# Performance work log

Measured on AMD Instinct MI355X. Metric: run time of the kernel, lower is better.

Reference implementation:

```python
import jax, jax.numpy as jnp
import numpy as np

B, N, C = 2, 384, 128
D = C // 4          # bottleneck_dim
H = 128             # time_mlp_hidden_dim


def setup_inputs() -> dict:
    key = jax.random.key(0)
    ks = jax.random.split(key, 12)
    s = 0.02
    return {
        "edge_embed": jax.random.normal(ks[0], (B, N, N, C), jnp.float32),
        "edge_mask": jax.random.randint(ks[1], (B, N, N), 0, 2, jnp.int32),
        "r3_t": jax.random.uniform(ks[2], (B,), jnp.float32),
        # linear params stored as [in, out]
        "Wg": jax.random.normal(ks[3], (C, D), jnp.float32) * s,
        "bg": jnp.zeros((D,), jnp.float32),
        "Wv": jax.random.normal(ks[4], (C, D), jnp.float32) * s,
        "bv": jnp.zeros((D,), jnp.float32),
        "Wd": jax.random.normal(ks[5], (C, D), jnp.float32) * s,
        "bd": jnp.zeros((D,), jnp.float32),
        "Wo": jax.random.normal(ks[6], (D, C), jnp.float32) * s,
        "bo": jnp.zeros((C,), jnp.float32),
        "W1": jax.random.normal(ks[7], (1, H), jnp.float32) * s,
        "b1": jnp.zeros((H,), jnp.float32),
        "W2": jax.random.normal(ks[8], (H, 2 * C), jnp.float32) * s,
        "b2": jnp.zeros((2 * C,), jnp.float32),
    }


def reference(edge_embed, edge_mask, r3_t, Wg, bg, Wv, bv, Wd, bd, Wo, bo, W1, b1, W2, b2):
    Bb, Nn, _, Cc = edge_embed.shape
    P = edge_embed.reshape(Bb, Nn * Nn, Cc)          # [B, N^2, C]
    m = (edge_mask.reshape(Bb, Nn * Nn, 1) != 0)
    mf = m.astype(P.dtype)

    fP = P @ Wg + bg                                 # [B, N^2, D]
    gP = P @ Wv + bv                                 # [B, N^2, D]
    fP = jnp.where(m, fP, jnp.asarray(-1e8, P.dtype))
    w = jax.nn.softmax(fP, axis=1)                   # softmax over all edges
    w = w * mf
    w = w / (w.sum(axis=1, keepdims=True) + 1e-8)

    V = jnp.einsum('bnd,bne->bde', w, gP)            # [B, D, D] global context

    hP = jax.nn.softmax(P @ Wd + bd, axis=2)         # softmax over channels
    O = jnp.einsum('bnd,bde->bne', hP, V)            # redistribute
    O = (O @ Wo + bo).reshape(Bb, Nn, Nn, Cc)

    # FiLM conditioned on timestep (torch GELU is exact erf form)
    t = r3_t.reshape(Bb, 1)
    t_emb = jax.nn.gelu(t @ W1 + b1, approximate=False) @ W2 + b2
    scale, shift = jnp.split(t_emb, 2, axis=-1)
    O = O * (1 + scale[:, None, None, :]) + shift[:, None, None, :]

    return edge_embed + O
```

## Files before the change

kernel.cpp:

```cpp
#include <hip/hip_runtime.h>
#include <hip/hip_bf16.h>
#include <math.h>

#define N2 147456
#define CC 128
#define TILES 2304

#define WS_VACC  0
#define WS_S     2048
#define WS_FS    2112
#define WS_SH    2368
#define WS_UPACK 2624
#define WS_B2P   6720

typedef __attribute__((ext_vector_type(8))) __bf16 bf16x8;
typedef __attribute__((ext_vector_type(4))) __bf16 bf16x4;
typedef __attribute__((ext_vector_type(4))) float f32x4;
typedef __attribute__((ext_vector_type(4))) short short4v;

#define MFMA16(a_, b_, c_) __builtin_amdgcn_mfma_f32_16x16x32_bf16((a_), (b_), (c_), 0, 0, 0)

static __device__ inline f32x4 mfma_k16(bf16x4 a, bf16x4 b, f32x4 c) {
#if __has_builtin(__builtin_amdgcn_mfma_f32_16x16x16_bf16)
    return __builtin_amdgcn_mfma_f32_16x16x16_bf16(a, b, c, 0, 0, 0);
#elif __has_builtin(__builtin_amdgcn_mfma_f32_16x16x16bf16_1k)
    return __builtin_amdgcn_mfma_f32_16x16x16bf16_1k(
        __builtin_bit_cast(short4v, a), __builtin_bit_cast(short4v, b), c, 0, 0, 0);
#else
    asm("v_mfma_f32_16x16x16_bf16 %0, %1, %2, %0" : "+v"(c) : "v"(a), "v"(b));
    return c;
#endif
}

__global__ __launch_bounds__(256) void k0_init(
    const float* __restrict__ r3t,
    const float* __restrict__ W1, const float* __restrict__ b1,
    const float* __restrict__ W2, const float* __restrict__ b2,
    float* __restrict__ ws)
{
    const int t = threadIdx.x, bx = blockIdx.x;
    if (bx > 0) {
        const int i = (bx - 1) * 256 + t;
        if (i < 2112) ws[i] = 0.0f;
        return;
    }
    __shared__ float h[2][128];
    {
        const int b = t >> 7, j = t & 127;
        const float x = r3t[b] * W1[j] + b1[j];
        h[b][j] = 0.5f * x * (1.0f + erff(x * 0.7071067811865475f));
    }
    __syncthreads();
    const int j2 = t;
    float acc0 = b2[j2], acc1 = b2[j2];
    for (int k = 0; k < 128; ++k) {
        const float w2 = W2[k * 256 + j2];
        acc0 += h[0][k] * w2;
        acc1 += h[1][k] * w2;
    }
    if (j2 < 128) {
        ws[WS_FS + j2]       = 1.0f + acc0;
        ws[WS_FS + 128 + j2] = 1.0f + acc1;
    } else {
        ws[WS_SH + (j2 - 128)]       = acc0;
        ws[WS_SH + 128 + (j2 - 128)] = acc1;
    }
}

__global__ __launch_bounds__(256, 3) void k1_accum(
    const float* __restrict__ P, const int* __restrict__ mask,
    const float* __restrict__ Wg, const float* __restrict__ bg,
    const float* __restrict__ Wv, const float* __restrict__ bv,
    float* __restrict__ ws)
{
    __shared__ float red[4][1024];
    __shared__ float red_s[4][32];

    const int t  = threadIdx.x;
    const int b  = blockIdx.y;
    const int w  = t >> 6;
    const int l  = t & 63;
    const int lr = l & 15;
    const int lg = l >> 4;

    bf16x8 wfrag[2][2][4];
    #pragma unroll
    for (int nt = 0; nt < 2; ++nt)
      #pragma unroll
      for (int ks = 0; ks < 4; ++ks) {
        const int base = (ks * 32 + 8 * lg) * 32 + nt * 16 + lr;
        bf16x8 f0, f1;
        #pragma unroll
        for (int i = 0; i < 8; ++i) {
            f0[i] = (__bf16)Wg[base + i * 32];
            f1[i] = (__bf16)Wv[base + i * 32];
        }
        wfrag[0][nt][ks] = f0;
        wfrag[1][nt][ks] = f1;
      }
    const float bgv[2] = { bg[lr], bg[lr + 16] };
    const float bvv[2] = { bv[lr], bv[lr + 16] };

    f32x4 vq00 = {0,0,0,0}, vq01 = {0,0,0,0}, vq10 = {0,0,0,0}, vq11 = {0,0,0,0};
    float s0 = 0.f, s1 = 0.f;

    const float* Pb = P + (size_t)b * N2 * CC;
    const int*   mb = mask + (size_t)b * N2;

    for (int tile = blockIdx.x; tile < TILES; tile += gridDim.x) {
        const int row0 = tile * 64 + w * 16;
        const float* prow = Pb + (size_t)(row0 + lr) * CC + 8 * lg;

        bf16x8 afrag[4];
        #pragma unroll
        for (int ks = 0; ks < 4; ++ks) {
            const float4 a0 = *(const float4*)(prow + ks * 32);
            const float4 a1 = *(const float4*)(prow + ks * 32 + 4);
            bf16x8 f;
            f[0] = (__bf16)a0.x; f[1] = (__bf16)a0.y; f[2] = (__bf16)a0.z; f[3] = (__bf16)a0.w;
            f[4] = (__bf16)a1.x; f[5] = (__bf16)a1.y; f[6] = (__bf16)a1.z; f[7] = (__bf16)a1.w;
            afrag[ks] = f;
        }

        f32x4 facc0 = {0,0,0,0}, facc1 = {0,0,0,0}, gacc0 = {0,0,0,0}, gacc1 = {0,0,0,0};
        #pragma unroll
        for (int ks = 0; ks < 4; ++ks) {
            facc0 = MFMA16(afrag[ks], wfrag[0][0][ks], facc0);
            facc1 = MFMA16(afrag[ks], wfrag[0][1][ks], facc1);
            gacc0 = MFMA16(afrag[ks], wfrag[1][0][ks], gacc0);
            gacc1 = MFMA16(afrag[ks], wfrag[1][1][ks], gacc1);
        }

        const int4 mk4 = *(const int4*)&mb[row0 + lg * 4];
        const int mk[4] = { mk4.x, mk4.y, mk4.z, mk4.w };

        bf16x4 pe0, pe1, pg0, pg1;
        #pragma unroll
        for (int r = 0; r < 4; ++r) {
            pe0[r] = (__bf16)(mk[r] ? __expf(facc0[r] + bgv[0]) : 0.0f);
            pe1[r] = (__bf16)(mk[r] ? __expf(facc1[r] + bgv[1]) : 0.0f);
            pg0[r] = (__bf16)(gacc0[r] + bvv[0]);
            pg1[r] = (__bf16)(gacc1[r] + bvv[1]);
        }

        #pragma unroll
        for (int r = 0; r < 4; ++r) {
            s0 += (float)pe0[r];
            s1 += (float)pe1[r];
        }

        vq00 = mfma_k16(pe0, pg0, vq00);
        vq01 = mfma_k16(pe0, pg1, vq01);
        vq10 = mfma_k16(pe1, pg0, vq10);
        vq11 = mfma_k16(pe1, pg1, vq11);
    }

    s0 += __shfl_xor(s0, 16); s0 += __shfl_xor(s0, 32);
    s1 += __shfl_xor(s1, 16); s1 += __shfl_xor(s1, 32);

    #pragma unroll
    for (int r = 0; r < 4; ++r) {
        red[w][(     4 * lg + r) * 32 +      lr] = vq00[r];
        red[w][(     4 * lg + r) * 32 + 16 + lr] = vq01[r];
        red[w][(16 + 4 * lg + r) * 32 +      lr] = vq10[r];
        red[w][(16 + 4 * lg + r) * 32 + 16 + lr] = vq11[r];
    }
    if (lg == 0) { red_s[w][lr] = s0; red_s[w][16 + lr] = s1; }
    __syncthreads();

    #pragma unroll
    for (int i = 0; i < 4; ++i) {
        const int idx = t + i * 256;
        const float v = red[0][idx] + red[1][idx] + red[2][idx] + red[3][idx];
        atomicAdd(ws + WS_VACC + b * 1024 + idx, v);
    }
    if (t < 32) {
        const float sv = red_s[0][t] + red_s[1][t] + red_s[2][t] + red_s[3][t];
        atomicAdd(ws + WS_S + b * 32 + t, sv);
    }
}

__global__ __launch_bounds__(256) void k2_mid(
    const float* __restrict__ Wo, const float* __restrict__ bo,
    float* __restrict__ ws)
{
    __shared__ float V[1024];
    __shared__ float wo[32][128];
    __shared__ float fs[128];
    const int t = threadIdx.x, b = blockIdx.x;

    if (t < 128) fs[t] = ws[WS_FS + b * 128 + t];
    #pragma unroll
    for (int i = 0; i < 4; ++i) {
        const int idx = t + i * 256;
        const int d = idx >> 5;
        const float s = ws[WS_S + b * 32 + d];
        V[idx] = ws[WS_VACC + b * 1024 + idx] / (s * (1.0f + 1e-8f));
    }
    #pragma unroll
    for (int i = 0; i < 4; ++i) {
        const int j = t + i * 256;
        ((float4*)&wo[0][0])[j] = ((const float4*)Wo)[j];
    }
    __syncthreads();

    const int c = t & 127, dh = t >> 7;
    float wcol[32];
    #pragma unroll
    for (int e = 0; e < 32; ++e) wcol[e] = wo[e][c];
    const float fsc = fs[c];
    if (dh == 0) ws[WS_B2P + b * 128 + c] = bo[c] * fsc + ws[WS_SH + b * 128 + c];

    __bf16* dst = (__bf16*)(ws + WS_UPACK);
    #pragma unroll
    for (int dd = 0; dd < 16; ++dd) {
        const int d = dh * 16 + dd;
        float acc = 0.0f;
        #pragma unroll
        for (int e = 0; e < 32; ++e) acc += V[d * 32 + e] * wcol[e];
        acc *= fsc;
        const int lg = d >> 3, ii = d & 7, nt = c >> 4, lr = c & 15;
        dst[(((size_t)b * 8 + nt) * 64 + (lg * 16 + lr)) * 8 + ii] = (__bf16)acc;
    }
}

__global__ __launch_bounds__(256, 3) void k3_out(
    const float* __restrict__ P,
    const float* __restrict__ Wd, const float* __restrict__ bd,
    const float* __restrict__ ws, float* __restrict__ out)
{
    __shared__ __bf16 h_t[64][40];

    const int t  = threadIdx.x;
    const int b  = blockIdx.y;
    const int w  = t >> 6, l = t & 63, lr = l & 15, lg = l >> 4;

    bf16x8 ufrag[8];
    {
        const bf16x8* up = (const bf16x8*)(ws + WS_UPACK) + (size_t)b * 512 + l;
        #pragma unroll
        for (int nt = 0; nt < 8; ++nt) ufrag[nt] = up[nt * 64];
    }
    float b2v[8][4];
    #pragma unroll
    for (int nt = 0; nt < 8; ++nt) {
        const float4 v = *(const float4*)(ws + WS_B2P + b * 128 + nt * 16 + lg * 4);
        b2v[nt][0] = v.x; b2v[nt][1] = v.y; b2v[nt][2] = v.z; b2v[nt][3] = v.w;
    }
    bf16x8 wdfrag[2][4];
    #pragma unroll
    for (int nt = 0; nt < 2; ++nt)
      #pragma unroll
      for (int ks = 0; ks < 4; ++ks) {
        const int base = (ks * 32 + 8 * lg) * 32 + nt * 16 + lr;
        bf16x8 f;
        #pragma unroll
        for (int i = 0; i < 8; ++i) f[i] = (__bf16)Wd[base + i * 32];
        wdfrag[nt][ks] = f;
      }
    float bdv[8];
    #pragma unroll
    for (int r = 0; r < 4; ++r) {
        bdv[r]     = bd[lg * 4 + r];
        bdv[4 + r] = bd[16 + lg * 4 + r];
    }

    const float* Pb = P + (size_t)b * N2 * CC;
    float*       Ob = out + (size_t)b * N2 * CC;

    for (int tile = TILES - 1 - blockIdx.x; tile >= 0; tile -= gridDim.x) {
        const int row0 = tile * 64 + w * 16;
        const size_t rbase = (size_t)(row0 + lr) * CC;
        const float* prow = Pb + rbase + 8 * lg;

        bf16x8 afrag[4];
        #pragma unroll
        for (int ks = 0; ks < 4; ++ks) {
            const float4 a0 = *(const float4*)(prow + ks * 32);
            const float4 a1 = *(const float4*)(prow + ks * 32 + 4);
            bf16x8 f;
            f[0] = (__bf16)a0.x; f[1] = (__bf16)a0.y; f[2] = (__bf16)a0.z; f[3] = (__bf16)a0.w;
            f[4] = (__bf16)a1.x; f[5] = (__bf16)a1.y; f[6] = (__bf16)a1.z; f[7] = (__bf16)a1.w;
            afrag[ks] = f;
        }
        float4 p4v[8];
        #pragma unroll
        for (int nt = 0; nt < 8; ++nt)
            p4v[nt] = *(const float4*)(Pb + rbase + nt * 16 + lg * 4);

        f32x4 dacc0 = {0,0,0,0}, dacc1 = {0,0,0,0};
        #pragma unroll
        for (int ks = 0; ks < 4; ++ks) {
            dacc0 = MFMA16(wdfrag[0][ks], afrag[ks], dacc0);
            dacc1 = MFMA16(wdfrag[1][ks], afrag[ks], dacc1);
        }

        float v[8];
        #pragma unroll
        for (int r = 0; r < 4; ++r) {
            v[r]     = dacc0[r] + bdv[r];
            v[4 + r] = dacc1[r] + bdv[4 + r];
        }
        float m = v[0];
        #pragma unroll
        for (int j = 1; j < 8; ++j) m = fmaxf(m, v[j]);
        m = fmaxf(m, __shfl_xor(m, 16));
        m = fmaxf(m, __shfl_xor(m, 32));
        float e[8], s = 0.f;
        #pragma unroll
        for (int j = 0; j < 8; ++j) { e[j] = __expf(v[j] - m); s += e[j]; }
        s += __shfl_xor(s, 16);
        s += __shfl_xor(s, 32);
        const float inv = 1.0f / s;

        bf16x4 h0, h1;
        #pragma unroll
        for (int r = 0; r < 4; ++r) {
            h0[r] = (__bf16)(e[r] * inv);
            h1[r] = (__bf16)(e[4 + r] * inv);
        }
        const int hrow = w * 16 + lr;
        *(bf16x4*)&h_t[hrow][lg * 4]      = h0;
        *(bf16x4*)&h_t[hrow][16 + lg * 4] = h1;
        const bf16x8 hf = *(const bf16x8*)&h_t[hrow][8 * lg];

        #pragma unroll
        for (int nt = 0; nt < 8; ++nt) {
            f32x4 ci;
            ci[0] = b2v[nt][0]; ci[1] = b2v[nt][1]; ci[2] = b2v[nt][2]; ci[3] = b2v[nt][3];
            const f32x4 oacc = MFMA16(ufrag[nt], hf, ci);
            const size_t off = rbase + nt * 16 + lg * 4;
            float4 o4;
            o4.x = p4v[nt].x + oacc[0]; o4.y = p4v[nt].y + oacc[1];
            o4.z = p4v[nt].z + oacc[2]; o4.w = p4v[nt].w + oacc[3];
            *(float4*)(Ob + off) = o4;
        }
    }
}

extern "C" void kernel_launch(void* const* d_in, const int* in_sizes, int n_in,
                              void* d_out, int out_size, void* d_ws, size_t ws_size,
                              hipStream_t stream) {
    const float* P   = (const float*)d_in[0];
    const int*   msk = (const int*)d_in[1];
    const float* r3t = (const float*)d_in[2];
    const float* Wg  = (const float*)d_in[3];
    const float* bg  = (const float*)d_in[4];
    const float* Wv  = (const float*)d_in[5];
    const float* bv  = (const float*)d_in[6];
    const float* Wd  = (const float*)d_in[7];
    const float* bd  = (const float*)d_in[8];
    const float* Wo  = (const float*)d_in[9];
    const float* bo  = (const float*)d_in[10];
    const float* W1  = (const float*)d_in[11];
    const float* b1  = (const float*)d_in[12];
    const float* W2  = (const float*)d_in[13];
    const float* b2  = (const float*)d_in[14];
    float* ws  = (float*)d_ws;
    float* out = (float*)d_out;

    hipLaunchKernelGGL(k0_init,  dim3(10),      dim3(256), 0, stream, r3t, W1, b1, W2, b2, ws);
    hipLaunchKernelGGL(k1_accum, dim3(384, 2),  dim3(256), 0, stream, P, msk, Wg, bg, Wv, bv, ws);
    hipLaunchKernelGGL(k2_mid,   dim3(2),       dim3(256), 0, stream, Wo, bo, ws);
    hipLaunchKernelGGL(k3_out,   dim3(768, 2),  dim3(256), 0, stream, P, Wd, bd, ws, out);
}
```

Baseline: 113.0 us.

## Compute channel softmax in first pass and stash bf16 result in output buffer

Moves the Wd projection and per-row channel softmax from the output kernel into the accumulation kernel, which already has the bf16 fragments of P loaded. The resulting bf16 h values are written into the start of each tile's region of the output buffer, and the output kernel reads them back instead of reloading P fragments and recomputing. The goal is to cut the second kernel's A-fragment loads and MFMA/softmax work, at the cost of extra global writes and reads of h and a __syncthreads so every wave has read h before the tile is overwritten.

```diff
diff --git a/kernel.cpp b/kernel.cpp
--- a/kernel.cpp
+++ b/kernel.cpp
@@ -71,7 +71,8 @@
     const float* __restrict__ P, const int* __restrict__ mask,
     const float* __restrict__ Wg, const float* __restrict__ bg,
     const float* __restrict__ Wv, const float* __restrict__ bv,
-    float* __restrict__ ws)
+    const float* __restrict__ Wd, const float* __restrict__ bd,
+    float* __restrict__ ws, float* __restrict__ out)
 {
     __shared__ float red[4][1024];
     __shared__ float red_s[4][32];
@@ -98,14 +99,32 @@
         wfrag[0][nt][ks] = f0;
         wfrag[1][nt][ks] = f1;
       }
+    bf16x8 wdfrag[2][4];
+    #pragma unroll
+    for (int nt = 0; nt < 2; ++nt)
+      #pragma unroll
+      for (int ks = 0; ks < 4; ++ks) {
+        const int base = (ks * 32 + 8 * lg) * 32 + nt * 16 + lr;
+        bf16x8 f;
+        #pragma unroll
+        for (int i = 0; i < 8; ++i) f[i] = (__bf16)Wd[base + i * 32];
+        wdfrag[nt][ks] = f;
+      }
     const float bgv[2] = { bg[lr], bg[lr + 16] };
     const float bvv[2] = { bv[lr], bv[lr + 16] };
+    float bdv[8];
+    #pragma unroll
+    for (int r = 0; r < 4; ++r) {
+        bdv[r]     = bd[lg * 4 + r];
+        bdv[4 + r] = bd[16 + lg * 4 + r];
+    }
 
     f32x4 vq00 = {0,0,0,0}, vq01 = {0,0,0,0}, vq10 = {0,0,0,0}, vq11 = {0,0,0,0};
     float s0 = 0.f, s1 = 0.f;
 
     const float* Pb = P + (size_t)b * N2 * CC;
     const int*   mb = mask + (size_t)b * N2;
+    float*       Ob = out + (size_t)b * N2 * CC;
 
     for (int tile = blockIdx.x; tile < TILES; tile += gridDim.x) {
         const int row0 = tile * 64 + w * 16;
@@ -120,6 +139,42 @@
             f[0] = (__bf16)a0.x; f[1] = (__bf16)a0.y; f[2] = (__bf16)a0.z; f[3] = (__bf16)a0.w;
             f[4] = (__bf16)a1.x; f[5] = (__bf16)a1.y; f[6] = (__bf16)a1.z; f[7] = (__bf16)a1.w;
             afrag[ks] = f;
+        }
+
+        {
+            f32x4 dacc0 = {0,0,0,0}, dacc1 = {0,0,0,0};
+            #pragma unroll
+            for (int ks = 0; ks < 4; ++ks) {
+                dacc0 = MFMA16(wdfrag[0][ks], afrag[ks], dacc0);
+                dacc1 = MFMA16(wdfrag[1][ks], afrag[ks], dacc1);
+            }
+            float v[8];
+            #pragma unroll
+            for (int r = 0; r < 4; ++r) {
+                v[r]     = dacc0[r] + bdv[r];
+                v[4 + r] = dacc1[r] + bdv[4 + r];
+            }
+            float m = v[0];
+            #pragma unroll
+            for (int j = 1; j < 8; ++j) m = fmaxf(m, v[j]);
+            m = fmaxf(m, __shfl_xor(m, 16));
+            m = fmaxf(m, __shfl_xor(m, 32));
+            float e[8], s = 0.f;
+            #pragma unroll
+            for (int j = 0; j < 8; ++j) { e[j] = __expf(v[j] - m); s += e[j]; }
+            s += __shfl_xor(s, 16);
+            s += __shfl_xor(s, 32);
+            const float inv = 1.0f / s;
+            bf16x4 h0, h1;
+            #pragma unroll
+            for (int r = 0; r < 4; ++r) {
+                h0[r] = (__bf16)(e[r] * inv);
+                h1[r] = (__bf16)(e[4 + r] * inv);
+            }
+            __bf16* hb = (__bf16*)(Ob + (size_t)tile * 8192);
+            const int R = w * 16 + lr;
+            *(bf16x4*)&hb[R * 32 + lg * 4]      = h0;
+            *(bf16x4*)&hb[R * 32 + 16 + lg * 4] = h1;
         }
 
         f32x4 facc0 = {0,0,0,0}, facc1 = {0,0,0,0}, gacc0 = {0,0,0,0}, gacc1 = {0,0,0,0};
@@ -226,11 +281,8 @@
 
 __global__ __launch_bounds__(256, 3) void k3_out(
     const float* __restrict__ P,
-    const float* __restrict__ Wd, const float* __restrict__ bd,
     const float* __restrict__ ws, float* __restrict__ out)
 {
-    __shared__ __bf16 h_t[64][40];
-
     const int t  = threadIdx.x;
     const int b  = blockIdx.y;
     const int w  = t >> 6, l = t & 63, lr = l & 15, lg = l >> 4;
@@ -247,23 +299,6 @@
         const float4 v = *(const float4*)(ws + WS_B2P + b * 128 + nt * 16 + lg * 4);
         b2v[nt][0] = v.x; b2v[nt][1] = v.y; b2v[nt][2] = v.z; b2v[nt][3] = v.w;
     }
-    bf16x8 wdfrag[2][4];
-    #pragma unroll
-    for (int nt = 0; nt < 2; ++nt)
-      #pragma unroll
-      for (int ks = 0; ks < 4; ++ks) {
-        const int base = (ks * 32 + 8 * lg) * 32 + nt * 16 + lr;
-        bf16x8 f;
-        #pragma unroll
-        for (int i = 0; i < 8; ++i) f[i] = (__bf16)Wd[base + i * 32];
-        wdfrag[nt][ks] = f;
-      }
-    float bdv[8];
-    #pragma unroll
-    for (int r = 0; r < 4; ++r) {
-        bdv[r]     = bd[lg * 4 + r];
-        bdv[4 + r] = bd[16 + lg * 4 + r];
-    }
 
     const float* Pb = P + (size_t)b * N2 * CC;
     float*       Ob = out + (size_t)b * N2 * CC;
@@ -271,58 +306,15 @@
     for (int tile = TILES - 1 - blockIdx.x; tile >= 0; tile -= gridDim.x) {
         const int row0 = tile * 64 + w * 16;
         const size_t rbase = (size_t)(row0 + lr) * CC;
-        const float* prow = Pb + rbase + 8 * lg;
-
-        bf16x8 afrag[4];
-        #pragma unroll
-        for (int ks = 0; ks < 4; ++ks) {
-            const float4 a0 = *(const float4*)(prow + ks * 32);
-            const float4 a1 = *(const float4*)(prow + ks * 32 + 4);
-            bf16x8 f;
-            f[0] = (__bf16)a0.x; f[1] = (__bf16)a0.y; f[2] = (__bf16)a0.z; f[3] = (__bf16)a0.w;
-            f[4] = (__bf16)a1.x; f[5] = (__bf16)a1.y; f[6] = (__bf16)a1.z; f[7] = (__bf16)a1.w;
-            afrag[ks] = f;
-        }
+
+        const __bf16* hb = (const __bf16*)(Ob + (size_t)tile * 8192);
+        const bf16x8 hf = *(const bf16x8*)&hb[(w * 16 + lr) * 32 + 8 * lg];
         float4 p4v[8];
         #pragma unroll
         for (int nt = 0; nt < 8; ++nt)
             p4v[nt] = *(const float4*)(Pb + rbase + nt * 16 + lg * 4);
 
-        f32x4 dacc0 = {0,0,0,0}, dacc1 = {0,0,0,0};
-        #pragma unroll
-        for (int ks = 0; ks < 4; ++ks) {
-            dacc0 = MFMA16(wdfrag[0][ks], afrag[ks], dacc0);
-            dacc1 = MFMA16(wdfrag[1][ks], afrag[ks], dacc1);
-        }
-
-        float v[8];
-        #pragma unroll
-        for (int r = 0; r < 4; ++r) {
-            v[r]     = dacc0[r] + bdv[r];
-            v[4 + r] = dacc1[r] + bdv[4 + r];
-        }
-        float m = v[0];
-        #pragma unroll
-        for (int j = 1; j < 8; ++j) m = fmaxf(m, v[j]);
-        m = fmaxf(m, __shfl_xor(m, 16));
-        m = fmaxf(m, __shfl_xor(m, 32));
-        float e[8], s = 0.f;
-        #pragma unroll
-        for (int j = 0; j < 8; ++j) { e[j] = __expf(v[j] - m); s += e[j]; }
-        s += __shfl_xor(s, 16);
-        s += __shfl_xor(s, 32);
-        const float inv = 1.0f / s;
-
-        bf16x4 h0, h1;
-        #pragma unroll
-        for (int r = 0; r < 4; ++r) {
-            h0[r] = (__bf16)(e[r] * inv);
-            h1[r] = (__bf16)(e[4 + r] * inv);
-        }
-        const int hrow = w * 16 + lr;
-        *(bf16x4*)&h_t[hrow][lg * 4]      = h0;
-        *(bf16x4*)&h_t[hrow][16 + lg * 4] = h1;
-        const bf16x8 hf = *(const bf16x8*)&h_t[hrow][8 * lg];
+        __syncthreads();
 
         #pragma unroll
         for (int nt = 0; nt < 8; ++nt) {
@@ -360,7 +352,7 @@
     float* out = (float*)d_out;
 
     hipLaunchKernelGGL(k0_init,  dim3(10),      dim3(256), 0, stream, r3t, W1, b1, W2, b2, ws);
-    hipLaunchKernelGGL(k1_accum, dim3(384, 2),  dim3(256), 0, stream, P, msk, Wg, bg, Wv, bv, ws);
+    hipLaunchKernelGGL(k1_accum, dim3(384, 2),  dim3(256), 0, stream, P, msk, Wg, bg, Wv, bv, Wd, bd, ws, out);
     hipLaunchKernelGGL(k2_mid,   dim3(2),       dim3(256), 0, stream, Wo, bo, ws);
-    hipLaunchKernelGGL(k3_out,   dim3(768, 2),  dim3(256), 0, stream, P, Wd, bd, ws, out);
-}
+    hipLaunchKernelGGL(k3_out,   dim3(768, 2),  dim3(256), 0, stream, P, ws, out);
+}
```

Measured after the change: 121.8 us. 7.8% more time.
